# Kernel optimization log

Measured on AMD Instinct MI355X. Metric: run time of the kernel, lower is better.

Reference implementation:

```python
import jax, jax.numpy as jnp
import numpy as np

N_HITS = 500_000
LATENT = 256
HITS_PER_TRACK = 10
NUM_TRACKS = N_HITS // HITS_PER_TRACK


def setup_inputs() -> dict:
    key = jax.random.key(0)
    k_h, k_w1, k_w2 = jax.random.split(key, 3)
    scale = 1.0 / np.sqrt(LATENT)
    h = jax.random.normal(k_h, (N_HITS, LATENT), dtype=jnp.float32)
    W1 = jax.random.normal(k_w1, (LATENT, LATENT), dtype=jnp.float32) * scale
    b1 = jnp.zeros((LATENT,), dtype=jnp.float32)
    w2 = jax.random.normal(k_w2, (LATENT,), dtype=jnp.float32) * scale
    b2 = jnp.zeros((), dtype=jnp.float32)
    # 10 hits per track, sorted, no empty segments
    batch_indices = (jnp.arange(N_HITS, dtype=jnp.int32) // HITS_PER_TRACK)
    return {"h": h, "W1": W1, "b1": b1, "w2": w2, "b2": b2,
            "batch_indices": batch_indices, "num_tracks": NUM_TRACKS}


def reference(h, W1, b1, w2, b2, batch_indices, num_tracks):
    # score_net: Linear -> Tanh -> Linear(->1), squeezed
    scores = jnp.tanh(h @ W1 + b1) @ w2 + b2            # (N,)
    # per-segment numerically-stable softmax
    seg_max = jax.ops.segment_max(scores, batch_indices, num_segments=num_tracks)
    e = jnp.exp(scores - seg_max[batch_indices])        # (N,)
    denom = jax.ops.segment_sum(e, batch_indices, num_segments=num_tracks)
    w = e / denom[batch_indices]                         # (N,)
    # per-segment weighted sum of h
    pooled = jax.ops.segment_sum(w[:, None] * h, batch_indices, num_segments=num_tracks)
    return pooled                                        # (num_tracks, LATENT)
```

## Files before the change

### kernel.cpp

```cpp
#include <hip/hip_runtime.h>
#include <hip/hip_bf16.h>


typedef __attribute__((ext_vector_type(8))) short short8;
typedef __attribute__((ext_vector_type(4))) float f32x4;

#define LATENT       256
#define HPT          10
#define TPB_TRACKS   40
#define ROWS_PB      (TPB_TRACKS * HPT)
#define STRIPS_PB    (ROWS_PB / 16)
#define WAVES        8
#define THREADS      (WAVES * 64)
#define W1_STRIDE    264
#define LOG2E        1.44269504088896f

__device__ __forceinline__ short bf16_rne(float x) {
    unsigned u = __float_as_uint(x);
    u += 0x7FFFu + ((u >> 16) & 1u);
    return (short)(u >> 16);
}

__device__ __forceinline__ float tanh_fast(float x) {
    float e = __builtin_amdgcn_exp2f(x * (2.0f * LOG2E));
    return 1.0f - 2.0f * __builtin_amdgcn_rcpf(e + 1.0f);
}

__global__ __launch_bounds__(THREADS, 2)
void softmax_pool_kernel(const float* __restrict__ h,
                         const float* __restrict__ W1,
                         const float* __restrict__ b1,
                         const float* __restrict__ w2,
                         float* __restrict__ out,
                         int n_hits, int num_tracks)
{
    __shared__ short w1t[256 * W1_STRIDE];
    __shared__ float sc_lds[ROWS_PB];

    const int tid  = threadIdx.x;
    const int wave = tid >> 6;
    const int lane = tid & 63;
    const int q    = lane >> 4;
    const int c    = lane & 15;
    const int blk  = blockIdx.x;

    for (int idx = tid; idx < 256 * 128; idx += THREADS) {
        int n = idx & 255;
        int k = (idx >> 8) << 1;
        float f0 = W1[(size_t)k * 256 + n];
        float f1 = W1[(size_t)(k + 1) * 256 + n];
        short2 p;
        p.x = bf16_rne(f0);
        p.y = bf16_rne(f1);
        *(short2*)&w1t[n * W1_STRIDE + k] = p;
    }
    __syncthreads();

    const int ns = (wave == 0) ? 4 : 3;

    short8 a[4][8] = {};
    #pragma unroll
    for (int st = 0; st < 4; ++st) {
        if (st < ns) {
            int strip = wave + st * 8;
            long row = (long)blk * ROWS_PB + strip * 16 + c;
            if (row >= n_hits) row = n_hits - 1;
            const float* hrow = h + (size_t)row * LATENT + q * 8;
            #pragma unroll
            for (int kt = 0; kt < 8; ++kt) {
                float4 f0 = *(const float4*)(hrow + kt * 32);
                float4 f1 = *(const float4*)(hrow + kt * 32 + 4);
                short8 v;
                v[0] = bf16_rne(f0.x); v[1] = bf16_rne(f0.y);
                v[2] = bf16_rne(f0.z); v[3] = bf16_rne(f0.w);
                v[4] = bf16_rne(f1.x); v[5] = bf16_rne(f1.y);
                v[6] = bf16_rne(f1.z); v[7] = bf16_rne(f1.w);
                a[st][kt] = v;
            }
        }
    }

    f32x4 zero4 = {0.0f, 0.0f, 0.0f, 0.0f};
    f32x4 sc[4] = {zero4, zero4, zero4, zero4};

    for (int ct = 0; ct < 16; ++ct) {
        int n = ct * 16 + c;
        const short* bbase = &w1t[n * W1_STRIDE + q * 8];
        f32x4 acc[4] = {zero4, zero4, zero4, zero4};
        #pragma unroll
        for (int kt = 0; kt < 8; ++kt) {
            short8 bf = *(const short8*)(bbase + kt * 32);
            #pragma unroll
            for (int st = 0; st < 4; ++st)
                if (st < ns)
                    acc[st] = __builtin_amdgcn_mfma_f32_16x16x32_bf16(a[st][kt], bf, acc[st], 0, 0, 0);
        }
        float b1n = b1[n];
        float w2n = w2[n];
        #pragma unroll
        for (int st = 0; st < 4; ++st) {
            if (st < ns) {
                #pragma unroll
                for (int r = 0; r < 4; ++r)
                    sc[st][r] += w2n * tanh_fast(acc[st][r] + b1n);
            }
        }
    }

    #pragma unroll
    for (int st = 0; st < 4; ++st) {
        #pragma unroll
        for (int r = 0; r < 4; ++r) {
            float v = sc[st][r];
            v += __shfl_xor(v, 1);
            v += __shfl_xor(v, 2);
            v += __shfl_xor(v, 4);
            v += __shfl_xor(v, 8);
            sc[st][r] = v;
        }
    }
    if (c == 0) {
        #pragma unroll
        for (int st = 0; st < 4; ++st) {
            if (st < ns) {
                int strip = wave + st * 8;
                float4 o;
                o.x = sc[st][0]; o.y = sc[st][1]; o.z = sc[st][2]; o.w = sc[st][3];
                *(float4*)&sc_lds[strip * 16 + q * 4] = o;
            }
        }
    }
    __syncthreads();

    if (tid < TPB_TRACKS) {
        float s[HPT];
        float m = -1e30f;
        #pragma unroll
        for (int i = 0; i < HPT; ++i) {
            s[i] = sc_lds[tid * HPT + i];
            m = fmaxf(m, s[i]);
        }
        float sum = 0.0f;
        #pragma unroll
        for (int i = 0; i < HPT; ++i) {
            s[i] = __builtin_amdgcn_exp2f((s[i] - m) * LOG2E);
            sum += s[i];
        }
        float inv = __builtin_amdgcn_rcpf(sum);
        #pragma unroll
        for (int i = 0; i < HPT; ++i)
            sc_lds[tid * HPT + i] = s[i] * inv;
    }
    __syncthreads();

    for (int t = wave; t < TPB_TRACKS; t += WAVES) {
        int tg = blk * TPB_TRACKS + t;
        if (tg >= num_tracks) continue;
        const float* hb = h + (size_t)tg * HPT * LATENT + lane * 4;
        float4 acc = {0.0f, 0.0f, 0.0f, 0.0f};
        #pragma unroll
        for (int i = 0; i < HPT; ++i) {
            float wi = sc_lds[t * HPT + i];
            float4 v = *(const float4*)(hb + (size_t)i * LATENT);
            acc.x += wi * v.x;
            acc.y += wi * v.y;
            acc.z += wi * v.z;
            acc.w += wi * v.w;
        }
        *(float4*)(out + (size_t)tg * LATENT + lane * 4) = acc;
    }
}

extern "C" void kernel_launch(void* const* d_in, const int* in_sizes, int n_in,
                              void* d_out, int out_size, void* d_ws, size_t ws_size,
                              hipStream_t stream) {
    const float* h  = (const float*)d_in[0];
    const float* W1 = (const float*)d_in[1];
    const float* b1 = (const float*)d_in[2];
    const float* w2 = (const float*)d_in[3];
    float* out = (float*)d_out;

    int n_hits     = in_sizes[0] / LATENT;
    int num_tracks = out_size / LATENT;
    int blocks     = (num_tracks + TPB_TRACKS - 1) / TPB_TRACKS;

    softmax_pool_kernel<<<blocks, THREADS, 0, stream>>>(h, W1, b1, w2, out, n_hits, num_tracks);
}
```

Baseline: 845.0 us.

## Pre-convert W1 to bf16 in workspace once and read B operand from global/L2

Moves the W1 transpose and bf16 conversion out of the main kernel into a separate small kernel that writes to the workspace. The main kernel drops its 132KB LDS W1 copy and reads B fragments straight from global memory, relying on L2 and cache reuse. Block size shrinks to 16 tracks with 5 waves, each handling 2 strips. This removes the per-block W1 staging cost and the LDS occupancy limit, at the price of more global B-fragment loads and smaller blocks.

```diff
diff --git a/kernel.cpp b/kernel.cpp
--- a/kernel.cpp
+++ b/kernel.cpp
@@ -1,5 +1,4 @@
 #include <hip/hip_runtime.h>
-#include <hip/hip_bf16.h>
 
 
 typedef __attribute__((ext_vector_type(8))) short short8;
@@ -7,12 +6,12 @@
 
 #define LATENT       256
 #define HPT          10
-#define TPB_TRACKS   40
+#define TPB_TRACKS   16
 #define ROWS_PB      (TPB_TRACKS * HPT)
 #define STRIPS_PB    (ROWS_PB / 16)
-#define WAVES        8
+#define WAVES        5
 #define THREADS      (WAVES * 64)
-#define W1_STRIDE    264
+#define NS           (STRIPS_PB / WAVES)
 #define LOG2E        1.44269504088896f
 
 __device__ __forceinline__ short bf16_rne(float x) {
@@ -26,15 +25,25 @@
     return 1.0f - 2.0f * __builtin_amdgcn_rcpf(e + 1.0f);
 }
 
-__global__ __launch_bounds__(THREADS, 2)
+__global__ __launch_bounds__(256)
+void convert_w1_kernel(const float* __restrict__ W1, short* __restrict__ w1t) {
+    int idx = blockIdx.x * 256 + threadIdx.x;
+    int n = idx & 255;
+    int k = (idx >> 8) << 1;
+    short2 p;
+    p.x = bf16_rne(W1[(size_t)k * LATENT + n]);
+    p.y = bf16_rne(W1[(size_t)(k + 1) * LATENT + n]);
+    *(short2*)&w1t[n * LATENT + k] = p;
+}
+
+__global__ __launch_bounds__(THREADS, 4)
 void softmax_pool_kernel(const float* __restrict__ h,
-                         const float* __restrict__ W1,
+                         const short* __restrict__ w1t,
                          const float* __restrict__ b1,
                          const float* __restrict__ w2,
                          float* __restrict__ out,
                          int n_hits, int num_tracks)
 {
-    __shared__ short w1t[256 * W1_STRIDE];
     __shared__ float sc_lds[ROWS_PB];
 
     const int tid  = threadIdx.x;
@@ -44,71 +53,53 @@
     const int c    = lane & 15;
     const int blk  = blockIdx.x;
 
-    for (int idx = tid; idx < 256 * 128; idx += THREADS) {
-        int n = idx & 255;
-        int k = (idx >> 8) << 1;
-        float f0 = W1[(size_t)k * 256 + n];
-        float f1 = W1[(size_t)(k + 1) * 256 + n];
-        short2 p;
-        p.x = bf16_rne(f0);
-        p.y = bf16_rne(f1);
-        *(short2*)&w1t[n * W1_STRIDE + k] = p;
-    }
-    __syncthreads();
-
-    const int ns = (wave == 0) ? 4 : 3;
-
-    short8 a[4][8] = {};
+    short8 a[NS][8];
     #pragma unroll
-    for (int st = 0; st < 4; ++st) {
-        if (st < ns) {
-            int strip = wave + st * 8;
-            long row = (long)blk * ROWS_PB + strip * 16 + c;
-            if (row >= n_hits) row = n_hits - 1;
-            const float* hrow = h + (size_t)row * LATENT + q * 8;
-            #pragma unroll
-            for (int kt = 0; kt < 8; ++kt) {
-                float4 f0 = *(const float4*)(hrow + kt * 32);
-                float4 f1 = *(const float4*)(hrow + kt * 32 + 4);
-                short8 v;
-                v[0] = bf16_rne(f0.x); v[1] = bf16_rne(f0.y);
-                v[2] = bf16_rne(f0.z); v[3] = bf16_rne(f0.w);
-                v[4] = bf16_rne(f1.x); v[5] = bf16_rne(f1.y);
-                v[6] = bf16_rne(f1.z); v[7] = bf16_rne(f1.w);
-                a[st][kt] = v;
-            }
+    for (int st = 0; st < NS; ++st) {
+        int strip = wave + st * WAVES;
+        long row = (long)blk * ROWS_PB + strip * 16 + c;
+        if (row >= n_hits) row = n_hits - 1;
+        const float* hrow = h + (size_t)row * LATENT + q * 8;
+        #pragma unroll
+        for (int kt = 0; kt < 8; ++kt) {
+            float4 f0 = *(const float4*)(hrow + kt * 32);
+            float4 f1 = *(const float4*)(hrow + kt * 32 + 4);
+            short8 v;
+            v[0] = bf16_rne(f0.x); v[1] = bf16_rne(f0.y);
+            v[2] = bf16_rne(f0.z); v[3] = bf16_rne(f0.w);
+            v[4] = bf16_rne(f1.x); v[5] = bf16_rne(f1.y);
+            v[6] = bf16_rne(f1.z); v[7] = bf16_rne(f1.w);
+            a[st][kt] = v;
         }
     }
 
     f32x4 zero4 = {0.0f, 0.0f, 0.0f, 0.0f};
-    f32x4 sc[4] = {zero4, zero4, zero4, zero4};
+    f32x4 sc[NS] = {zero4, zero4};
 
+    #pragma unroll 1
     for (int ct = 0; ct < 16; ++ct) {
         int n = ct * 16 + c;
-        const short* bbase = &w1t[n * W1_STRIDE + q * 8];
-        f32x4 acc[4] = {zero4, zero4, zero4, zero4};
+        float b1n = b1[n];
+        float w2n = w2[n];
+        const short* bbase = w1t + n * LATENT + q * 8;
+        f32x4 acc[NS] = {zero4, zero4};
         #pragma unroll
         for (int kt = 0; kt < 8; ++kt) {
             short8 bf = *(const short8*)(bbase + kt * 32);
             #pragma unroll
-            for (int st = 0; st < 4; ++st)
-                if (st < ns)
-                    acc[st] = __builtin_amdgcn_mfma_f32_16x16x32_bf16(a[st][kt], bf, acc[st], 0, 0, 0);
+            for (int st = 0; st < NS; ++st)
+                acc[st] = __builtin_amdgcn_mfma_f32_16x16x32_bf16(a[st][kt], bf, acc[st], 0, 0, 0);
         }
-        float b1n = b1[n];
-        float w2n = w2[n];
         #pragma unroll
-        for (int st = 0; st < 4; ++st) {
-            if (st < ns) {
-                #pragma unroll
-                for (int r = 0; r < 4; ++r)
-                    sc[st][r] += w2n * tanh_fast(acc[st][r] + b1n);
-            }
+        for (int st = 0; st < NS; ++st) {
+            #pragma unroll
+            for (int r = 0; r < 4; ++r)
+                sc[st][r] += w2n * tanh_fast(acc[st][r] + b1n);
         }
     }
 
     #pragma unroll
-    for (int st = 0; st < 4; ++st) {
+    for (int st = 0; st < NS; ++st) {
         #pragma unroll
         for (int r = 0; r < 4; ++r) {
             float v = sc[st][r];
@@ -121,35 +112,36 @@
     }
     if (c == 0) {
         #pragma unroll
-        for (int st = 0; st < 4; ++st) {
-            if (st < ns) {
-                int strip = wave + st * 8;
-                float4 o;
-                o.x = sc[st][0]; o.y = sc[st][1]; o.z = sc[st][2]; o.w = sc[st][3];
-                *(float4*)&sc_lds[strip * 16 + q * 4] = o;
-            }
+        for (int st = 0; st < NS; ++st) {
+            int strip = wave + st * WAVES;
+            float4 o;
+            o.x = sc[st][0]; o.y = sc[st][1]; o.z = sc[st][2]; o.w = sc[st][3];
+            *(float4*)&sc_lds[strip * 16 + q * 4] = o;
         }
     }
     __syncthreads();
 
     if (tid < TPB_TRACKS) {
-        float s[HPT];
-        float m = -1e30f;
-        #pragma unroll
-        for (int i = 0; i < HPT; ++i) {
-            s[i] = sc_lds[tid * HPT + i];
-            m = fmaxf(m, s[i]);
+        int tg = blk * TPB_TRACKS + tid;
+        if (tg < num_tracks) {
+            float s[HPT];
+            float m = -1e30f;
+            #pragma unroll
+            for (int i = 0; i < HPT; ++i) {
+                s[i] = sc_lds[tid * HPT + i];
+                m = fmaxf(m, s[i]);
+            }
+            float sum = 0.0f;
+            #pragma unroll
+            for (int i = 0; i < HPT; ++i) {
+                s[i] = __builtin_amdgcn_exp2f((s[i] - m) * LOG2E);
+                sum += s[i];
+            }
+            float inv = __builtin_amdgcn_rcpf(sum);
+            #pragma unroll
+            for (int i = 0; i < HPT; ++i)
+                sc_lds[tid * HPT + i] = s[i] * inv;
         }
-        float sum = 0.0f;
-        #pragma unroll
-        for (int i = 0; i < HPT; ++i) {
-            s[i] = __builtin_amdgcn_exp2f((s[i] - m) * LOG2E);
-            sum += s[i];
-        }
-        float inv = __builtin_amdgcn_rcpf(sum);
-        #pragma unroll
-        for (int i = 0; i < HPT; ++i)
-            sc_lds[tid * HPT + i] = s[i] * inv;
     }
     __syncthreads();
 
@@ -179,10 +171,13 @@
     const float* b1 = (const float*)d_in[2];
     const float* w2 = (const float*)d_in[3];
     float* out = (float*)d_out;
+    short* w1t = (short*)d_ws;
 
     int n_hits     = in_sizes[0] / LATENT;
     int num_tracks = out_size / LATENT;
     int blocks     = (num_tracks + TPB_TRACKS - 1) / TPB_TRACKS;
 
-    softmax_pool_kernel<<<blocks, THREADS, 0, stream>>>(h, W1, b1, w2, out, n_hits, num_tracks);
+    convert_w1_kernel<<<128, 256, 0, stream>>>(W1, w1t);
+    softmax_pool_kernel<<<blocks, THREADS, 0, stream>>>(h, w1t, b1, w2, out,
+                                                        n_hits, num_tracks);
 }
```

New measurement: 947.3 us. +12.1%, slower.
